# Kernel tuning notes

Hardware: AMD Instinct MI355X
Metric: run time of the kernel (lower is better)

## Reference

```python
import jax, jax.numpy as jnp
import numpy as np

NUM_HEADS = 4
EPS = 1e-5


def conv1(W, b, z):
    # Conv1d with kernel_size=1 == channel-wise linear: (B, Cin, L) -> (B, Cout, L)
    return jnp.einsum('oi,bil->bol', W, z) + b[None, :, None]


def setup_inputs() -> dict:
    key = jax.random.key(0)
    ks = jax.random.split(key, 16)
    B, D, N = 2, 256, 4096
    s = 0.05
    return {
        'x': jax.random.normal(ks[0], (B, D, N), jnp.float32),
        'source': jax.random.normal(ks[1], (B, D, N), jnp.float32),
        'Wq': jax.random.normal(ks[2], (D, D), jnp.float32) * s,
        'bq': jax.random.normal(ks[3], (D,), jnp.float32) * s,
        'Wk': jax.random.normal(ks[4], (D, D), jnp.float32) * s,
        'bk': jax.random.normal(ks[5], (D,), jnp.float32) * s,
        'Wv': jax.random.normal(ks[6], (D, D), jnp.float32) * s,
        'bv': jax.random.normal(ks[7], (D,), jnp.float32) * s,
        'Wm': jax.random.normal(ks[8], (D, D), jnp.float32) * s,
        'bm': jax.random.normal(ks[9], (D,), jnp.float32) * s,
        'W1': jax.random.normal(ks[10], (2 * D, 2 * D), jnp.float32) * s,
        'b1': jax.random.normal(ks[11], (2 * D,), jnp.float32) * s,
        'W2': jax.random.normal(ks[12], (D, 2 * D), jnp.float32) * s,
        'b2': jax.random.normal(ks[13], (D,), jnp.float32) * s,
    }


def reference(x, source, Wq, bq, Wk, bk, Wv, bv, Wm, bm, W1, b1, W2, b2):
    B, D, N = x.shape
    M = source.shape[2]
    H = NUM_HEADS
    dim = D // H  # per-head dim; torch reshape splits channels as (dim, heads)

    q = conv1(Wq, bq, x).reshape(B, dim, H, N)
    k = conv1(Wk, bk, source).reshape(B, dim, H, M)
    v = conv1(Wv, bv, source).reshape(B, dim, H, M)

    scores = jnp.einsum('bdhn,bdhm->bhnm', q, k) / (dim ** 0.5)
    prob = jax.nn.softmax(scores, axis=-1)
    attn = jnp.einsum('bhnm,bdhm->bdhn', prob, v).reshape(B, D, N)

    message = conv1(Wm, bm, attn)

    h = conv1(W1, b1, jnp.concatenate([x, message], axis=1))
    # InstanceNorm1d (affine=False, biased var over L)
    mu = jnp.mean(h, axis=2, keepdims=True)
    var = jnp.mean((h - mu) ** 2, axis=2, keepdims=True)
    h = jax.nn.relu((h - mu) / jnp.sqrt(var + EPS))
    return conv1(W2, b2, h)
```

## Files before the change

### kernel.cpp

```cpp
#include <hip/hip_runtime.h>
#include <cstdint>
#include <cstddef>


typedef __attribute__((ext_vector_type(8))) short short8;
typedef __attribute__((ext_vector_type(4))) float floatx4;

union U4 { unsigned int u[4]; short8 s; };

__device__ __forceinline__ unsigned short f2bf(float x) {
  union { float f; unsigned int u; } c; c.f = x;
  unsigned int r = c.u + 0x7FFFu + ((c.u >> 16) & 1u);
  return (unsigned short)(r >> 16);
}
__device__ __forceinline__ float bf2f(unsigned short u) {
  union { unsigned int i; float f; } c; c.i = ((unsigned int)u) << 16; return c.f;
}
__device__ __forceinline__ void gload16(const void* g, void* l) {
  __builtin_amdgcn_global_load_lds(
      (const __attribute__((address_space(1))) unsigned int*)g,
      (__attribute__((address_space(3))) unsigned int*)l, 16, 0, 0);
}
__device__ __forceinline__ unsigned int cvtpk(float lo, float hi) {
  unsigned int r;
  asm("v_cvt_pk_bf16_f32 %0, %1, %2" : "=v"(r) : "v"(lo), "v"(hi));
  return r;
}

#define LOG2E_8 0.18033688011112042f

__global__ __launch_bounds__(256) void tx_all(
    const float* __restrict__ x, const float* __restrict__ src,
    unsigned short* __restrict__ xb, unsigned short* __restrict__ sb,
    int C, int N)
{
  __shared__ float tile[32][33];
  const int which = blockIdx.z >> 1, b = blockIdx.z & 1;
  const float* X = which ? src : x;
  unsigned short* Y = which ? sb : xb;
  const int n0 = blockIdx.x * 32, c0 = blockIdx.y * 32;
  const int tc = threadIdx.x & 31, tr = threadIdx.x >> 5;
  #pragma unroll
  for (int i = 0; i < 4; ++i)
    tile[tr + i * 8][tc] = X[((size_t)b * C + c0 + tr + i * 8) * N + n0 + tc];
  __syncthreads();
  #pragma unroll
  for (int i = 0; i < 4; ++i)
    Y[((size_t)b * N + n0 + tr + i * 8) * C + c0 + tc] = f2bf(tile[tc][tr + i * 8]);
}

__global__ __launch_bounds__(256) void wprep(
    const float* __restrict__ Wq, const float* __restrict__ Wk,
    const float* __restrict__ Wv, const float* __restrict__ Wm,
    const float* __restrict__ W1, const float* __restrict__ W2,
    const float* __restrict__ bq, const float* __restrict__ bk,
    const float* __restrict__ bv, const float* __restrict__ bm,
    const float* __restrict__ b1, const float* __restrict__ b2,
    unsigned short* __restrict__ wqkv, unsigned short* __restrict__ wm_,
    unsigned short* __restrict__ w1_, unsigned short* __restrict__ w2_,
    float* __restrict__ biasb)
{
  const int bid = blockIdx.x, t = threadIdx.x;
  if (bid < 768) {
    const int idx = bid * 256 + t;
    const int op = idx >> 8, ip = idx & 255;
    const int grp = op >> 8, oo = op & 255;
    const int o = 4 * (oo & 63) + (oo >> 6);
    const float* W = grp == 0 ? Wq : grp == 1 ? Wk : Wv;
    const float sc = grp == 0 ? LOG2E_8 : 1.f;
    wqkv[idx] = f2bf(W[(size_t)o * 256 + ip] * sc);
  } else if (bid < 1024) {
    const int idx = (bid - 768) * 256 + t;
    const int op = idx >> 8, ip = idx & 255;
    const int i2 = 4 * (ip & 63) + (ip >> 6);
    wm_[idx] = f2bf(Wm[(size_t)op * 256 + i2]);
  } else if (bid < 2048) {
    const int idx = (bid - 1024) * 256 + t;
    w1_[idx] = f2bf(W1[idx]);
  } else if (bid < 2560) {
    const int idx = (bid - 2048) * 256 + t;
    w2_[idx] = f2bf(W2[idx]);
  } else {
    const int z = (bid - 2560) * 256 + t;
    if (z < 256)       biasb[z] = bq[4 * (z & 63) + (z >> 6)] * LOG2E_8;
    else if (z < 512)  { const int y = z - 256; biasb[z] = bk[4 * (y & 63) + (y >> 6)]; }
    else if (z < 768)  { const int y = z - 512; biasb[z] = bv[4 * (y & 63) + (y >> 6)]; }
    else if (z < 1024) biasb[z] = bm[z - 768];
    else if (z < 1536) biasb[z] = b1[z - 1024];
    else if (z < 1792) biasb[z] = b2[z - 1536];
  }
}

template<int BN>
__global__ __launch_bounds__(256) void gemmT(
    const unsigned short* __restrict__ Wb, const float* __restrict__ bias,
    const unsigned short* __restrict__ X0, const unsigned short* __restrict__ X1,
    void* __restrict__ O0, void* __restrict__ O1, void* __restrict__ O2,
    int Co, int Ci, int Ci0, int N, int variant)
{
  constexpr int NJ = BN / 32;
  const int n0 = blockIdx.x * BN;
  const int o0 = blockIdx.y * 64;
  const int b  = blockIdx.z;
  const int t  = threadIdx.x;
  const int w = t >> 6, lane = t & 63, qd = lane >> 4, l = lane & 15;
  const int oh = (w >> 1) * 32, nh = (w & 1) * (BN / 2);

  __shared__ unsigned short Wl[64 * 64];
  __shared__ unsigned short Xl[BN * 64];

  floatx4 acc[2][NJ];
  #pragma unroll
  for (int i = 0; i < 2; ++i)
    #pragma unroll
    for (int j = 0; j < NJ; ++j) acc[i][j] = (floatx4){0.f, 0.f, 0.f, 0.f};

  for (int k0 = 0; k0 < Ci; k0 += 64) {
    const unsigned short* Xs; int cb, rl;
    if (variant == 1) { Xs = (o0 < 256) ? X0 : X1; cb = k0; rl = Ci; }
    else if (k0 < Ci0) { Xs = X0; cb = k0; rl = Ci0; }
    else               { Xs = X1; cb = k0 - Ci0; rl = Ci - Ci0; }
    __syncthreads();
    #pragma unroll
    for (int i = 0; i < 2; ++i) {
      const int idx = i * 256 + t;
      const int row = idx >> 3, pg = idx & 7, sg = pg ^ (row & 7);
      gload16(&Wb[(size_t)(o0 + row) * Ci + k0 + sg * 8], &Wl[row * 64 + pg * 8]);
    }
    #pragma unroll
    for (int i = 0; i < BN / 32; ++i) {
      const int idx = i * 256 + t;
      const int row = idx >> 3, pg = idx & 7, sg = pg ^ (row & 7);
      gload16(&Xs[((size_t)b * N + n0 + row) * rl + cb + sg * 8], &Xl[row * 64 + pg * 8]);
    }
    __syncthreads();

    short8 af[2][2], bf[NJ][2];
    #pragma unroll
    for (int i = 0; i < 2; ++i) {
      const int ar = oh + 16 * i + l;
      af[i][0] = *(const short8*)&Wl[ar * 64 + ((qd ^ (ar & 7))) * 8];
      af[i][1] = *(const short8*)&Wl[ar * 64 + (((4 + qd) ^ (ar & 7))) * 8];
    }
    #pragma unroll
    for (int j = 0; j < NJ; ++j) {
      const int br = nh + 16 * j + l;
      bf[j][0] = *(const short8*)&Xl[br * 64 + ((qd ^ (br & 7))) * 8];
      bf[j][1] = *(const short8*)&Xl[br * 64 + (((4 + qd) ^ (br & 7))) * 8];
    }
    #pragma unroll
    for (int i = 0; i < 2; ++i)
      #pragma unroll
      for (int j = 0; j < NJ; ++j) {
        acc[i][j] = __builtin_amdgcn_mfma_f32_16x16x32_bf16(af[i][0], bf[j][0], acc[i][j], 0, 0, 0);
        acc[i][j] = __builtin_amdgcn_mfma_f32_16x16x32_bf16(af[i][1], bf[j][1], acc[i][j], 0, 0, 0);
      }
  }

  const int osec = o0 + oh;
  #pragma unroll
  for (int i = 0; i < 2; ++i) {
    const int o4 = o0 + oh + 16 * i + qd * 4;
    const float4 bi = *(const float4*)&bias[o4];
    #pragma unroll
    for (int j = 0; j < NJ; ++j) {
      const int n = n0 + nh + 16 * j + l;
      if (variant == 0) {
        unsigned short* C = (unsigned short*)O0;
        ushort4 pk;
        pk.x = f2bf(acc[i][j][0] + bi.x); pk.y = f2bf(acc[i][j][1] + bi.y);
        pk.z = f2bf(acc[i][j][2] + bi.z); pk.w = f2bf(acc[i][j][3] + bi.w);
        *(ushort4*)&C[((size_t)b * N + n) * Co + o4] = pk;
      } else if (variant == 1) {
        if (osec < 256) {
          unsigned short* C = (unsigned short*)O0;
          ushort4 pk;
          pk.x = f2bf(acc[i][j][0] + bi.x); pk.y = f2bf(acc[i][j][1] + bi.y);
          pk.z = f2bf(acc[i][j][2] + bi.z); pk.w = f2bf(acc[i][j][3] + bi.w);
          *(ushort4*)&C[((size_t)b * N + n) * 256 + o4] = pk;
        } else if (osec < 512) {
          unsigned short* C = (unsigned short*)O1;
          ushort4 pk;
          pk.x = f2bf(acc[i][j][0] + bi.x); pk.y = f2bf(acc[i][j][1] + bi.y);
          pk.z = f2bf(acc[i][j][2] + bi.z); pk.w = f2bf(acc[i][j][3] + bi.w);
          *(ushort4*)&C[((size_t)b * N + n) * 256 + (o4 - 256)] = pk;
        } else {
          unsigned short* C = (unsigned short*)O2;
          #pragma unroll
          for (int rg = 0; rg < 4; ++rg) {
            const int op = o4 - 512 + rg, h = op >> 6, d = op & 63;
            C[(((size_t)b * 4 + h) * 64 + d) * N + n] =
                f2bf(acc[i][j][rg] + ((const float*)&bi)[rg]);
          }
        }
      } else {
        float* C = (float*)O0;
        #pragma unroll
        for (int rg = 0; rg < 4; ++rg)
          C[((size_t)b * Co + o4 + rg) * N + n] = acc[i][j][rg] + ((const float*)&bi)[rg];
      }
    }
  }
}

__global__ __launch_bounds__(256) void attn_mfma(
    const unsigned short* __restrict__ qb, const unsigned short* __restrict__ kb,
    const unsigned short* __restrict__ vh, unsigned short* __restrict__ Opart,
    float* __restrict__ liPart, int N)
{
  const int qt = blockIdx.x;
  const int h  = blockIdx.y;
  const int b  = blockIdx.z >> 2, s = blockIdx.z & 3;
  const int n0 = qt * 128;
  const int t  = threadIdx.x;
  const int w = t >> 6, lane = t & 63, qd = lane >> 4, l = lane & 15;

  __shared__ unsigned short Kl[2][64 * 64];
  __shared__ unsigned short Vl[2][64 * 64];

  const unsigned short* qp0 = &qb[((size_t)b * N + n0 + 16 * w + l) * 256 + h * 64];
  const unsigned short* qp1 = qp0 + (size_t)64 * 256;
  short8 bQ[2][2];
  bQ[0][0] = *(const short8*)&qp0[qd * 8];
  bQ[0][1] = *(const short8*)&qp0[32 + qd * 8];
  bQ[1][0] = *(const short8*)&qp1[qd * 8];
  bQ[1][1] = *(const short8*)&qp1[32 + qd * 8];

  short8 ones;
  #pragma unroll
  for (int i = 0; i < 8; ++i) ones[i] = (short)0x3F80;

  floatx4 accO[2][4];
  floatx4 accLi[2];
  #pragma unroll
  for (int qs = 0; qs < 2; ++qs) {
    accLi[qs] = (floatx4){0.f, 0.f, 0.f, 0.f};
    #pragma unroll
    for (int ds = 0; ds < 4; ++ds) accO[qs][ds] = (floatx4){0.f, 0.f, 0.f, 0.f};
  }

  const int j0base = s * 1024;

  auto STAGE = [&](int buf, int j0) {
    #pragma unroll
    for (int i = 0; i < 2; ++i) {
      const int idx = i * 256 + t;
      const int row = idx >> 3, pg = idx & 7, sg = pg ^ (row & 7);
      gload16(&kb[((size_t)b * N + j0 + row) * 256 + h * 64 + sg * 8],
              &Kl[buf][row * 64 + pg * 8]);
      gload16(&vh[(((size_t)b * 4 + h) * 64 + row) * N + j0 + sg * 8],
              &Vl[buf][row * 64 + pg * 8]);
    }
  };

  STAGE(0, j0base);

  #pragma unroll 2
  for (int jt = 0; jt < 16; ++jt) {
    const int cur = jt & 1;
    __syncthreads();
    if (jt < 15) STAGE(cur ^ 1, j0base + (jt + 1) * 64);

    floatx4 S[2][4];
    __builtin_amdgcn_s_setprio(1);
    #pragma unroll
    for (int js = 0; js < 4; ++js) {
      const int br = 16 * js + l;
      const short8 k0 = *(const short8*)&Kl[cur][br * 64 + ((qd ^ (br & 7))) * 8];
      const short8 k1 = *(const short8*)&Kl[cur][br * 64 + (((4 + qd) ^ (br & 7))) * 8];
      floatx4 a0 = (floatx4){0.f, 0.f, 0.f, 0.f};
      floatx4 a1 = (floatx4){0.f, 0.f, 0.f, 0.f};
      a0 = __builtin_amdgcn_mfma_f32_16x16x32_bf16(k0, bQ[0][0], a0, 0, 0, 0);
      a1 = __builtin_amdgcn_mfma_f32_16x16x32_bf16(k0, bQ[1][0], a1, 0, 0, 0);
      a0 = __builtin_amdgcn_mfma_f32_16x16x32_bf16(k1, bQ[0][1], a0, 0, 0, 0);
      a1 = __builtin_amdgcn_mfma_f32_16x16x32_bf16(k1, bQ[1][1], a1, 0, 0, 0);
      S[0][js] = a0; S[1][js] = a1;
    }
    __builtin_amdgcn_s_setprio(0);

    unsigned int T[2][2][4];
    #pragma unroll
    for (int qs = 0; qs < 2; ++qs) {
      unsigned int U[4], W[4];
      #pragma unroll
      for (int js = 0; js < 4; ++js) {
        const float p0 = __builtin_exp2f(S[qs][js][0]);
        const float p1 = __builtin_exp2f(S[qs][js][1]);
        const float p2 = __builtin_exp2f(S[qs][js][2]);
        const float p3 = __builtin_exp2f(S[qs][js][3]);
        U[js] = cvtpk(p0, p1);
        W[js] = cvtpk(p2, p3);
      }
      #pragma unroll
      for (int js2 = 0; js2 < 2; ++js2) {
        unsigned int t0 = U[2 * js2], t2 = U[2 * js2 + 1];
        asm("v_permlane32_swap_b32 %0, %1" : "+v"(t0), "+v"(t2));
        asm("v_permlane16_swap_b32 %0, %1" : "+v"(t0), "+v"(t2));
        unsigned int t1 = W[2 * js2], t3 = W[2 * js2 + 1];
        asm("v_permlane32_swap_b32 %0, %1" : "+v"(t1), "+v"(t3));
        asm("v_permlane16_swap_b32 %0, %1" : "+v"(t1), "+v"(t3));
        T[qs][js2][0] = t0; T[qs][js2][1] = t1;
        T[qs][js2][2] = t2; T[qs][js2][3] = t3;
      }
    }

    __builtin_amdgcn_s_setprio(1);
    #pragma unroll
    for (int js2 = 0; js2 < 2; ++js2) {
      short8 vv[4];
      #pragma unroll
      for (int ds = 0; ds < 4; ++ds) {
        const int vr = 16 * ds + l;
        vv[ds] = *(const short8*)&Vl[cur][vr * 64 + (((4 * js2 + qd) ^ (vr & 7))) * 8];
      }
      #pragma unroll
      for (int qs = 0; qs < 2; ++qs) {
        U4 pu;
        pu.u[0] = T[qs][js2][0]; pu.u[1] = T[qs][js2][1];
        pu.u[2] = T[qs][js2][2]; pu.u[3] = T[qs][js2][3];
        const short8 pa = pu.s;
        #pragma unroll
        for (int ds = 0; ds < 4; ++ds)
          accO[qs][ds] = __builtin_amdgcn_mfma_f32_16x16x32_bf16(pa, vv[ds], accO[qs][ds], 0, 0, 0);
        accLi[qs] = __builtin_amdgcn_mfma_f32_16x16x32_bf16(pa, ones, accLi[qs], 0, 0, 0);
      }
    }
    __builtin_amdgcn_s_setprio(0);
  }

  const size_t obase = ((((size_t)b * 4 + h) * 4 + s) * 32 + qt) * 128;
  #pragma unroll
  for (int qs = 0; qs < 2; ++qs)
    #pragma unroll
    for (int rg = 0; rg < 4; ++rg) {
      const int q = qs * 64 + 16 * w + qd * 4 + rg;
      #pragma unroll
      for (int ds = 0; ds < 4; ++ds)
        Opart[(obase + q) * 64 + 16 * ds + l] = f2bf(accO[qs][ds][rg]);
      if (l == 0) liPart[obase + q] = accLi[qs][rg];
    }
}

__global__ __launch_bounds__(256) void attn_combine(
    const unsigned short* __restrict__ Opart, const float* __restrict__ liPart,
    unsigned short* __restrict__ atb, int N)
{
  const int qt = blockIdx.x, h = blockIdx.y, b = blockIdx.z;
  const int t = threadIdx.x;
  const int q = t >> 1, d0 = (t & 1) * 32;

  float li = 0.f;
  size_t idx[4];
  #pragma unroll
  for (int s = 0; s < 4; ++s) {
    idx[s] = ((((size_t)b * 4 + h) * 4 + s) * 32 + qt) * 128 + q;
    li += liPart[idx[s]];
  }
  const float inv = 1.f / li;

  float o[32];
  #pragma unroll
  for (int c = 0; c < 32; ++c) o[c] = 0.f;
  #pragma unroll
  for (int s = 0; s < 4; ++s) {
    #pragma unroll
    for (int c4 = 0; c4 < 4; ++c4) {
      const short8 v = *(const short8*)&Opart[idx[s] * 64 + d0 + c4 * 8];
      #pragma unroll
      for (int j = 0; j < 8; ++j) o[c4 * 8 + j] += bf2f((unsigned short)v[j]);
    }
  }
  unsigned short* dst = &atb[((size_t)b * N + qt * 128 + q) * 256 + h * 64 + d0];
  #pragma unroll
  for (int c4 = 0; c4 < 4; ++c4) {
    ushort4 pk;
    pk.x = f2bf(o[c4 * 8 + 0] * inv); pk.y = f2bf(o[c4 * 8 + 1] * inv);
    pk.z = f2bf(o[c4 * 8 + 2] * inv); pk.w = f2bf(o[c4 * 8 + 3] * inv);
    *(ushort4*)&dst[c4 * 8] = pk;
    pk.x = f2bf(o[c4 * 8 + 4] * inv); pk.y = f2bf(o[c4 * 8 + 5] * inv);
    pk.z = f2bf(o[c4 * 8 + 6] * inv); pk.w = f2bf(o[c4 * 8 + 7] * inv);
    *(ushort4*)&dst[c4 * 8 + 4] = pk;
  }
}

__global__ __launch_bounds__(256) void in_stats(
    const unsigned short* __restrict__ H, float* __restrict__ Ps,
    float* __restrict__ Ps2, int N)
{
  const int cg = blockIdx.x, ns = blockIdx.y, b = blockIdx.z, t = threadIdx.x;
  const int c0 = cg * 64 + (t & 7) * 8;
  float s[8] = {}, s2[8] = {};
  #pragma unroll
  for (int i = 0; i < 8; ++i) {
    const int n = ns * 256 + (t >> 3) + i * 32;
    const short8 hv = *(const short8*)&H[((size_t)b * N + n) * 512 + c0];
    #pragma unroll
    for (int j = 0; j < 8; ++j) {
      const float f = bf2f((unsigned short)hv[j]);
      s[j] += f; s2[j] += f * f;
    }
  }
  __shared__ float rs[32][64], rs2[32][64];
  #pragma unroll
  for (int j = 0; j < 8; ++j) {
    rs[t >> 3][(t & 7) * 8 + j] = s[j];
    rs2[t >> 3][(t & 7) * 8 + j] = s2[j];
  }
  __syncthreads();
  if (t < 64) {
    float a = 0.f, a2 = 0.f;
    #pragma unroll
    for (int r = 0; r < 32; ++r) { a += rs[r][t]; a2 += rs2[r][t]; }
    const size_t o = ((size_t)ns * 2 + b) * 512 + cg * 64 + t;
    Ps[o] = a; Ps2[o] = a2;
  }
}

__global__ __launch_bounds__(256) void in_norm(
    unsigned short* __restrict__ H, const float* __restrict__ Ps,
    const float* __restrict__ Ps2, int N)
{
  const int cg = blockIdx.x, ns = blockIdx.y, b = blockIdx.z, t = threadIdx.x;
  __shared__ float muS[64], ivS[64];
  if (t < 64) {
    const int c = cg * 64 + t;
    float s = 0.f, s2 = 0.f;
    for (int k = 0; k < 16; ++k) {
      s  += Ps [((size_t)k * 2 + b) * 512 + c];
      s2 += Ps2[((size_t)k * 2 + b) * 512 + c];
    }
    const float mu = s / (float)N;
    const float var = fmaxf(s2 / (float)N - mu * mu, 0.f);
    muS[t] = mu;
    ivS[t] = rsqrtf(var + 1e-5f);
  }
  __syncthreads();
  const int c0 = cg * 64 + (t & 7) * 8;
  float mu[8], iv[8];
  #pragma unroll
  for (int j = 0; j < 8; ++j) {
    mu[j] = muS[(t & 7) * 8 + j];
    iv[j] = ivS[(t & 7) * 8 + j];
  }
  #pragma unroll
  for (int i = 0; i < 8; ++i) {
    const int n = ns * 256 + (t >> 3) + i * 32;
    unsigned short* p = &H[((size_t)b * N + n) * 512 + c0];
    short8 hv = *(const short8*)p;
    #pragma unroll
    for (int j = 0; j < 8; ++j) {
      const float f = fmaxf((bf2f((unsigned short)hv[j]) - mu[j]) * iv[j], 0.f);
      hv[j] = (short)f2bf(f);
    }
    *(short8*)p = hv;
  }
}

extern "C" void kernel_launch(void* const* d_in, const int* in_sizes, int n_in,
                              void* d_out, int out_size, void* d_ws, size_t ws_size,
                              hipStream_t stream)
{
  const int B = 2, D = 256, N = 4096;

  const float* x   = (const float*)d_in[0];
  const float* src = (const float*)d_in[1];
  const float* Wq  = (const float*)d_in[2];  const float* bq = (const float*)d_in[3];
  const float* Wk  = (const float*)d_in[4];  const float* bk = (const float*)d_in[5];
  const float* Wv  = (const float*)d_in[6];  const float* bv = (const float*)d_in[7];
  const float* Wm  = (const float*)d_in[8];  const float* bm = (const float*)d_in[9];
  const float* W1  = (const float*)d_in[10]; const float* b1 = (const float*)d_in[11];
  const float* W2  = (const float*)d_in[12]; const float* b2 = (const float*)d_in[13];
  float* out = (float*)d_out;

  char* ws = (char*)d_ws;
  const size_t MB = 1u << 20;
  unsigned short* xb  = (unsigned short*)(ws + 0 * MB);
  unsigned short* sb  = (unsigned short*)(ws + 4 * MB);
  unsigned short* qbf = (unsigned short*)(ws + 8 * MB);
  unsigned short* kbf = (unsigned short*)(ws + 12 * MB);
  unsigned short* vhb = (unsigned short*)(ws + 16 * MB);
  unsigned short* atb = (unsigned short*)(ws + 20 * MB);
  unsigned short* Opart = (unsigned short*)(ws + 24 * MB);
  unsigned short* msb = (unsigned short*)(ws + 24 * MB);
  unsigned short* hb  = (unsigned short*)(ws + 28 * MB);
  float* liPart = (float*)(ws + 41 * MB);
  unsigned short* wqkvb = (unsigned short*)(ws + 42 * MB);
  unsigned short* wmb = wqkvb + 768 * 256;
  unsigned short* w1b = wmb + 256 * 256;
  unsigned short* w2b = w1b + 512 * 512;
  float* biasb = (float*)(ws + 44 * MB);
  float* Ps    = biasb + 2048;
  float* Ps2   = Ps + 16 * 2 * 512;

  const dim3 blk(256);

  tx_all<<<dim3(N / 32, D / 32, 2 * B), blk, 0, stream>>>(x, src, xb, sb, D, N);
  wprep<<<dim3(2567), blk, 0, stream>>>(Wq, Wk, Wv, Wm, W1, W2,
                                        bq, bk, bv, bm, b1, b2,
                                        wqkvb, wmb, w1b, w2b, biasb);

  gemmT<128><<<dim3(N / 128, 12, B), blk, 0, stream>>>(
      wqkvb, biasb, xb, sb, qbf, kbf, vhb, 768, 256, 256, N, 1);

  attn_mfma<<<dim3(N / 128, 4, B * 4), blk, 0, stream>>>(
      qbf, kbf, vhb, Opart, liPart, N);
  attn_combine<<<dim3(N / 128, 4, B), blk, 0, stream>>>(Opart, liPart, atb, N);

  gemmT<64><<<dim3(N / 64, 4, B), blk, 0, stream>>>(
      wmb, biasb + 768, atb, atb, msb, nullptr, nullptr, 256, 256, 256, N, 0);

  gemmT<64><<<dim3(N / 64, 8, B), blk, 0, stream>>>(
      w1b, biasb + 1024, xb, msb, hb, nullptr, nullptr, 512, 512, 256, N, 0);

  in_stats<<<dim3(8, 16, B), blk, 0, stream>>>(hb, Ps, Ps2, N);
  in_norm<<<dim3(8, 16, B), blk, 0, stream>>>(hb, Ps, Ps2, N);

  gemmT<64><<<dim3(N / 64, 4, B), blk, 0, stream>>>(
      w2b, biasb + 1536, hb, hb, out, nullptr, nullptr, 256, 512, 512, N, 2);
}
```

Baseline: 209.7 us.

## Fuse instance-norm apply and ReLU into final GEMM operand load

Removes the separate in_norm pass, which read and rewrote the whole hidden activation buffer. The final GEMM instead computes per-channel scale and shift from accumulated statistics and applies normalisation and ReLU to B-fragments in registers before the MFMA. The stats kernel now reduces with atomicAdd into per-batch totals, which are zeroed by an extra block in the weight-prep kernel. This adds ALU and LDS work inside the GEMM inner loop and makes the float sums order-nondeterministic.

```diff
diff --git a/kernel.cpp b/kernel.cpp
--- a/kernel.cpp
+++ b/kernel.cpp
@@ -58,7 +58,8 @@
     const float* __restrict__ b1, const float* __restrict__ b2,
     unsigned short* __restrict__ wqkv, unsigned short* __restrict__ wm_,
     unsigned short* __restrict__ w1_, unsigned short* __restrict__ w2_,
-    float* __restrict__ biasb)
+    float* __restrict__ biasb, float* __restrict__ PsT,
+    float* __restrict__ Ps2T)
 {
   const int bid = blockIdx.x, t = threadIdx.x;
   if (bid < 768) {
@@ -80,7 +81,7 @@
   } else if (bid < 2560) {
     const int idx = (bid - 2048) * 256 + t;
     w2_[idx] = f2bf(W2[idx]);
-  } else {
+  } else if (bid < 2567) {
     const int z = (bid - 2560) * 256 + t;
     if (z < 256)       biasb[z] = bq[4 * (z & 63) + (z >> 6)] * LOG2E_8;
     else if (z < 512)  { const int y = z - 256; biasb[z] = bk[4 * (y & 63) + (y >> 6)]; }
@@ -88,14 +89,21 @@
     else if (z < 1024) biasb[z] = bm[z - 768];
     else if (z < 1536) biasb[z] = b1[z - 1024];
     else if (z < 1792) biasb[z] = b2[z - 1536];
-  }
-}
-
-template<int BN>
+  } else {
+    #pragma unroll
+    for (int k = 0; k < 4; ++k) {
+      PsT[k * 256 + t] = 0.f;
+      Ps2T[k * 256 + t] = 0.f;
+    }
+  }
+}
+
+template<int BN, bool NRM>
 __global__ __launch_bounds__(256) void gemmT(
     const unsigned short* __restrict__ Wb, const float* __restrict__ bias,
     const unsigned short* __restrict__ X0, const unsigned short* __restrict__ X1,
     void* __restrict__ O0, void* __restrict__ O1, void* __restrict__ O2,
+    const float* __restrict__ PsT, const float* __restrict__ Ps2T,
     int Co, int Ci, int Ci0, int N, int variant)
 {
   constexpr int NJ = BN / 32;
@@ -108,6 +116,21 @@
 
   __shared__ unsigned short Wl[64 * 64];
   __shared__ unsigned short Xl[BN * 64];
+  __shared__ float aS[NRM ? 512 : 1];
+  __shared__ float bS[NRM ? 512 : 1];
+
+  if constexpr (NRM) {
+    const float invN = 1.f / (float)N;
+    for (int c = t; c < Ci; c += 256) {
+      const float s  = PsT [(size_t)b * Ci + c];
+      const float s2 = Ps2T[(size_t)b * Ci + c];
+      const float mu = s * invN;
+      const float var = fmaxf(s2 * invN - mu * mu, 0.f);
+      const float iv = rsqrtf(var + 1e-5f);
+      aS[c] = iv;
+      bS[c] = -mu * iv;
+    }
+  }
 
   floatx4 acc[2][NJ];
   #pragma unroll
@@ -147,6 +170,25 @@
       const int br = nh + 16 * j + l;
       bf[j][0] = *(const short8*)&Xl[br * 64 + ((qd ^ (br & 7))) * 8];
       bf[j][1] = *(const short8*)&Xl[br * 64 + (((4 + qd) ^ (br & 7))) * 8];
+    }
+    if constexpr (NRM) {
+      #pragma unroll
+      for (int j = 0; j < NJ; ++j)
+        #pragma unroll
+        for (int hh = 0; hh < 2; ++hh) {
+          const int cc = k0 + (hh * 4 + qd) * 8;
+          const short8 v = bf[j][hh];
+          U4 pu;
+          #pragma unroll
+          for (int e = 0; e < 4; ++e) {
+            const float f0 = fmaxf(
+                fmaf(bf2f((unsigned short)v[2 * e]), aS[cc + 2 * e], bS[cc + 2 * e]), 0.f);
+            const float f1 = fmaxf(
+                fmaf(bf2f((unsigned short)v[2 * e + 1]), aS[cc + 2 * e + 1], bS[cc + 2 * e + 1]), 0.f);
+            pu.u[e] = cvtpk(f0, f1);
+          }
+          bf[j][hh] = pu.s;
+        }
     }
     #pragma unroll
     for (int i = 0; i < 2; ++i)
@@ -384,8 +426,8 @@
 }
 
 __global__ __launch_bounds__(256) void in_stats(
-    const unsigned short* __restrict__ H, float* __restrict__ Ps,
-    float* __restrict__ Ps2, int N)
+    const unsigned short* __restrict__ H, float* __restrict__ PsT,
+    float* __restrict__ Ps2T, int N)
 {
   const int cg = blockIdx.x, ns = blockIdx.y, b = blockIdx.z, t = threadIdx.x;
   const int c0 = cg * 64 + (t & 7) * 8;
@@ -411,48 +453,9 @@
     float a = 0.f, a2 = 0.f;
     #pragma unroll
     for (int r = 0; r < 32; ++r) { a += rs[r][t]; a2 += rs2[r][t]; }
-    const size_t o = ((size_t)ns * 2 + b) * 512 + cg * 64 + t;
-    Ps[o] = a; Ps2[o] = a2;
-  }
-}
-
-__global__ __launch_bounds__(256) void in_norm(
-    unsigned short* __restrict__ H, const float* __restrict__ Ps,
-    const float* __restrict__ Ps2, int N)
-{
-  const int cg = blockIdx.x, ns = blockIdx.y, b = blockIdx.z, t = threadIdx.x;
-  __shared__ float muS[64], ivS[64];
-  if (t < 64) {
     const int c = cg * 64 + t;
-    float s = 0.f, s2 = 0.f;
-    for (int k = 0; k < 16; ++k) {
-      s  += Ps [((size_t)k * 2 + b) * 512 + c];
-      s2 += Ps2[((size_t)k * 2 + b) * 512 + c];
-    }
-    const float mu = s / (float)N;
-    const float var = fmaxf(s2 / (float)N - mu * mu, 0.f);
-    muS[t] = mu;
-    ivS[t] = rsqrtf(var + 1e-5f);
-  }
-  __syncthreads();
-  const int c0 = cg * 64 + (t & 7) * 8;
-  float mu[8], iv[8];
-  #pragma unroll
-  for (int j = 0; j < 8; ++j) {
-    mu[j] = muS[(t & 7) * 8 + j];
-    iv[j] = ivS[(t & 7) * 8 + j];
-  }
-  #pragma unroll
-  for (int i = 0; i < 8; ++i) {
-    const int n = ns * 256 + (t >> 3) + i * 32;
-    unsigned short* p = &H[((size_t)b * N + n) * 512 + c0];
-    short8 hv = *(const short8*)p;
-    #pragma unroll
-    for (int j = 0; j < 8; ++j) {
-      const float f = fmaxf((bf2f((unsigned short)hv[j]) - mu[j]) * iv[j], 0.f);
-      hv[j] = (short)f2bf(f);
-    }
-    *(short8*)p = hv;
+    atomicAdd(&PsT [(size_t)b * 512 + c], a);
+    atomicAdd(&Ps2T[(size_t)b * 512 + c], a2);
   }
 }
 
@@ -489,32 +492,34 @@
   unsigned short* w1b = wmb + 256 * 256;
   unsigned short* w2b = w1b + 512 * 512;
   float* biasb = (float*)(ws + 44 * MB);
-  float* Ps    = biasb + 2048;
-  float* Ps2   = Ps + 16 * 2 * 512;
+  float* PsT   = biasb + 2048;
+  float* Ps2T  = PsT + 1024;
 
   const dim3 blk(256);
 
   tx_all<<<dim3(N / 32, D / 32, 2 * B), blk, 0, stream>>>(x, src, xb, sb, D, N);
-  wprep<<<dim3(2567), blk, 0, stream>>>(Wq, Wk, Wv, Wm, W1, W2,
+  wprep<<<dim3(2568), blk, 0, stream>>>(Wq, Wk, Wv, Wm, W1, W2,
                                         bq, bk, bv, bm, b1, b2,
-                                        wqkvb, wmb, w1b, w2b, biasb);
-
-  gemmT<128><<<dim3(N / 128, 12, B), blk, 0, stream>>>(
-      wqkvb, biasb, xb, sb, qbf, kbf, vhb, 768, 256, 256, N, 1);
+                                        wqkvb, wmb, w1b, w2b, biasb, PsT, Ps2T);
+
+  gemmT<128, false><<<dim3(N / 128, 12, B), blk, 0, stream>>>(
+      wqkvb, biasb, xb, sb, qbf, kbf, vhb, nullptr, nullptr, 768, 256, 256, N, 1);
 
   attn_mfma<<<dim3(N / 128, 4, B * 4), blk, 0, stream>>>(
       qbf, kbf, vhb, Opart, liPart, N);
   attn_combine<<<dim3(N / 128, 4, B), blk, 0, stream>>>(Opart, liPart, atb, N);
 
-  gemmT<64><<<dim3(N / 64, 4, B), blk, 0, stream>>>(
-      wmb, biasb + 768, atb, atb, msb, nullptr, nullptr, 256, 256, 256, N, 0);
-
-  gemmT<64><<<dim3(N / 64, 8, B), blk, 0, stream>>>(
-      w1b, biasb + 1024, xb, msb, hb, nullptr, nullptr, 512, 512, 256, N, 0);
-
-  in_stats<<<dim3(8, 16, B), blk, 0, stream>>>(hb, Ps, Ps2, N);
-  in_norm<<<dim3(8, 16, B), blk, 0, stream>>>(hb, Ps, Ps2, N);
-
-  gemmT<64><<<dim3(N / 64, 4, B), blk, 0, stream>>>(
-      w2b, biasb + 1536, hb, hb, out, nullptr, nullptr, 256, 512, 512, N, 2);
-}
+  gemmT<64, false><<<dim3(N / 64, 4, B), blk, 0, stream>>>(
+      wmb, biasb + 768, atb, atb, msb, nullptr, nullptr, nullptr, nullptr,
+      256, 256, 256, N, 0);
+
+  gemmT<64, false><<<dim3(N / 64, 8, B), blk, 0, stream>>>(
+      w1b, biasb + 1024, xb, msb, hb, nullptr, nullptr, nullptr, nullptr,
+      512, 512, 256, N, 0);
+
+  in_stats<<<dim3(8, 16, B), blk, 0, stream>>>(hb, PsT, Ps2T, N);
+
+  gemmT<64, true><<<dim3(N / 64, 4, B), blk, 0, stream>>>(
+      w2b, biasb + 1536, hb, hb, out, nullptr, nullptr, PsT, Ps2T,
+      256, 512, 512, N, 2);
+}
```

Result: no change. 205.8 us (-1.8%).
